# Optimization experiments

Measured on AMD Instinct MI355X. Metric: run time of the kernel, lower is better.

The kernel has to match this reference:

```python
import jax, jax.numpy as jnp
import numpy as np

B = 2048          # number of graphs
NPG = 128         # nodes per graph (hard-coded by lin1 = Linear(128*hid, 1))
N = B * NPG       # total nodes = 262144
DEG = 16          # avg degree
EPG = NPG * DEG   # edges per graph
E = B * EPG       # total edges = 4194304
IN_CH = 151
HID = 64


def setup_inputs() -> dict:
    key = jax.random.key(0)
    ks = jax.random.split(key, 6)
    x = jax.random.normal(ks[0], (N, IN_CH), jnp.float32)
    # within-graph random edges: local index in [0, NPG) plus per-graph node offset
    src_loc = jax.random.randint(ks[1], (E,), 0, NPG, dtype=jnp.int32)
    dst_loc = jax.random.randint(ks[2], (E,), 0, NPG, dtype=jnp.int32)
    off = ((jnp.arange(E, dtype=jnp.int32) // EPG) * NPG)
    edge_index = jnp.stack([src_loc + off, dst_loc + off])  # [2, E] int32
    edge_weight = jax.random.uniform(ks[3], (E,), jnp.float32)
    batch = jnp.arange(N, dtype=jnp.int32) // NPG  # sorted graph ids
    W1 = jax.random.normal(ks[4], (IN_CH, HID), jnp.float32) / np.sqrt(IN_CH)
    b1 = jnp.zeros((HID,), jnp.float32)
    Wlin = jax.random.normal(ks[5], (NPG * HID, 1), jnp.float32) / np.sqrt(NPG * HID)
    blin = jnp.zeros((1,), jnp.float32)
    return {"x": x, "edge_index": edge_index, "edge_weight": edge_weight,
            "batch": batch, "W1": W1, "b1": b1, "Wlin": Wlin, "blin": blin}


def _gcn_conv(x, row, col, w, W, b, num_nodes):
    # PyG GCNConv: h = x @ W; out[col] += dinv[row]*w*dinv[col] * h[row]; out += b
    h = x @ W                                        # [N, HID]
    deg = jax.ops.segment_sum(w, col, num_segments=num_nodes)
    dinv = jnp.where(deg > 0, jax.lax.rsqrt(deg), 0.0)
    norm = dinv[row] * w * dinv[col]                 # [E+N]
    out = jax.ops.segment_sum(h[row] * norm[:, None], col, num_segments=num_nodes)
    return out + b


def reference(x, edge_index, edge_weight, batch, W1, b1, Wlin, blin):
    num_nodes = x.shape[0]
    # add self-loops with weight 1 (GCNConv default)
    sl = jnp.arange(num_nodes, dtype=edge_index.dtype)
    row = jnp.concatenate([edge_index[0], sl])
    col = jnp.concatenate([edge_index[1], sl])
    w = jnp.concatenate([edge_weight, jnp.ones((num_nodes,), x.dtype)])
    h = jax.nn.relu(_gcn_conv(x, row, col, w, W1, b1, num_nodes))  # [N, HID]
    # linearize: nodes are batch-sorted, 128 per graph -> [B, 128*HID]
    g = h.reshape(num_nodes // NPG, NPG * h.shape[1])
    return jax.nn.sigmoid(g @ Wlin + blin)  # [B, 1]
```

## Files before the change

kernel.cpp:

```cpp
#include <hip/hip_runtime.h>
#include <math.h>

#define NPG 128
#define HID 64
#define ICH 151
#define EPG 2048
#define TPB 512
#define EPT (EPG / TPB)
#define KP  160
#define HTS 136
#define ASS 132
#define AS_OFF 17408

typedef __attribute__((ext_vector_type(8))) short  short8;
typedef __attribute__((ext_vector_type(4))) float  floatx4;

static __device__ __forceinline__ unsigned short f2bf(float v) {
    unsigned u = __builtin_bit_cast(unsigned, v);
    return (unsigned short)((u + 0x7fffu + ((u >> 16) & 1u)) >> 16);
}
static __device__ __forceinline__ unsigned packbf(float a, float b) {
    return (unsigned)f2bf(a) | ((unsigned)f2bf(b) << 16);
}
static __device__ __forceinline__ short8 pack8(const float* v) {
    union { unsigned u[4]; short8 s; } r;
    r.u[0] = packbf(v[0], v[1]);
    r.u[1] = packbf(v[2], v[3]);
    r.u[2] = packbf(v[4], v[5]);
    r.u[3] = packbf(v[6], v[7]);
    return r.s;
}

__global__ __launch_bounds__(512) void gcn_prep(const float* __restrict__ W1,
                                                short* __restrict__ W1T) {
    int i = threadIdx.x + blockIdx.x * 512;
    if (i < HID * KP) {
        int ch = i / KP, k = i - ch * KP;
        W1T[i] = (short)f2bf((k < ICH) ? W1[k * HID + ch] : 0.0f);
    }
}

__global__ __launch_bounds__(TPB, 6) void gcn_fused(
    const float* __restrict__ x,
    const int*   __restrict__ erow,
    const int*   __restrict__ ecol,
    const float* __restrict__ ew,
    const short* __restrict__ W1T,
    const float* __restrict__ b1,
    const float* __restrict__ Wlin,
    const float* __restrict__ blin,
    float* __restrict__ out)
{
    __shared__ __align__(16) char smem[AS_OFF + 64 * ASS * 4];
    __shared__ float deg[NPG];
    __shared__ float dinv[NPG];
    __shared__ float red[TPB / 64];

    short* ht = (short*)smem;
    float* As = (float*)(smem + AS_OFF);

    const int t    = threadIdx.x;
    const int g    = blockIdx.x;
    const int lane = t & 63;
    const int wv   = t >> 6;
    const int c16  = lane & 15;
    const int kq   = (lane >> 4) * 8;

    if (t < NPG) deg[t] = 1.0f;

    int   ep_[EPT];
    float nw_[EPT];
    const int ebase = g * EPG;
    #pragma unroll
    for (int it = 0; it < EPT; ++it) {
        int e = ebase + t + it * TPB;
        int rl = erow[e] & (NPG - 1);
        int cl = ecol[e] & (NPG - 1);
        ep_[it] = (cl << 7) | rl;
        nw_[it] = ew[e];
    }

    short8 af[5];
    {
        const float* xr = x + (size_t)g * (NPG * ICH) + (wv * 16 + c16) * ICH;
        #pragma unroll
        for (int s = 0; s < 5; ++s) {
            float v[8];
            #pragma unroll
            for (int j = 0; j < 8; ++j) {
                int k = s * 32 + kq + j;
                v[j] = (k < ICH) ? xr[k] : 0.0f;
            }
            af[s] = pack8(v);
        }
    }
    __syncthreads();

    #pragma unroll
    for (int it = 0; it < EPT; ++it)
        atomicAdd(&deg[ep_[it] >> 7], nw_[it]);

    #pragma unroll
    for (int n = 0; n < 4; ++n) {
        floatx4 acc = {0.0f, 0.0f, 0.0f, 0.0f};
        #pragma unroll
        for (int s = 0; s < 5; ++s) {
            short8 b = *(const short8*)&W1T[(n * 16 + c16) * KP + s * 32 + kq];
            acc = __builtin_amdgcn_mfma_f32_16x16x32_bf16(af[s], b, acc, 0, 0, 0);
        }
        int col = n * 16 + c16;
        int row = wv * 16 + (lane >> 4) * 4;
        *(int2*)&ht[col * HTS + row] =
            make_int2((int)packbf(acc[0], acc[1]), (int)packbf(acc[2], acc[3]));
    }
    __syncthreads();

    if (t < NPG) dinv[t] = rsqrtf(deg[t]);
    __syncthreads();

    #pragma unroll
    for (int it = 0; it < EPT; ++it) {
        int rl = ep_[it] & (NPG - 1), cl = ep_[it] >> 7;
        nw_[it] = dinv[rl] * nw_[it] * dinv[cl];
    }

    float partial = 0.0f;
    const int mrow = (wv >> 1) * 16 + c16;

    for (int half = 0; half < 2; ++half) {
        for (int p = t; p < 64 * ASS / 4; p += TPB)
            ((floatx4*)As)[p] = (floatx4){0.0f, 0.0f, 0.0f, 0.0f};
        __syncthreads();

        #pragma unroll
        for (int it = 0; it < EPT; ++it) {
            int cl = ep_[it] >> 7;
            if ((cl >> 6) == half)
                atomicAdd(&As[(cl & 63) * ASS + (ep_[it] & (NPG - 1))], nw_[it]);
        }
        if (t < 64) {
            int i = half * 64 + t;
            atomicAdd(&As[t * ASS + i], dinv[i] * dinv[i]);
        }
        __syncthreads();

        short8 afr[4];
        #pragma unroll
        for (int ks = 0; ks < 4; ++ks) {
            const float* ap = &As[mrow * ASS + ks * 32 + kq];
            floatx4 a0 = *(const floatx4*)ap;
            floatx4 a1 = *(const floatx4*)(ap + 4);
            float v[8] = {a0[0], a0[1], a0[2], a0[3], a1[0], a1[1], a1[2], a1[3]};
            afr[ks] = pack8(v);
        }
        #pragma unroll
        for (int nn = 0; nn < 2; ++nn) {
            int nt2 = (wv & 1) * 2 + nn;
            floatx4 acc = {0.0f, 0.0f, 0.0f, 0.0f};
            #pragma unroll
            for (int ks = 0; ks < 4; ++ks) {
                short8 b = *(const short8*)&ht[(nt2 * 16 + c16) * HTS + ks * 32 + kq];
                acc = __builtin_amdgcn_mfma_f32_16x16x32_bf16(afr[ks], b, acc, 0, 0, 0);
            }
            int col = nt2 * 16 + c16;
            float b1v = b1[col];
            int node0 = half * 64 + (wv >> 1) * 16 + (lane >> 4) * 4;
            #pragma unroll
            for (int r = 0; r < 4; ++r) {
                float v = fmaxf(acc[r] + b1v, 0.0f);
                partial += v * Wlin[(node0 + r) * HID + col];
            }
        }
        __syncthreads();
    }

    #pragma unroll
    for (int o = 32; o > 0; o >>= 1)
        partial += __shfl_down(partial, o, 64);
    if (lane == 0) red[wv] = partial;
    __syncthreads();
    if (t == 0) {
        float tot = blin[0];
        #pragma unroll
        for (int i = 0; i < TPB / 64; ++i) tot += red[i];
        out[g] = 1.0f / (1.0f + expf(-tot));
    }
}

extern "C" void kernel_launch(void* const* d_in, const int* in_sizes, int n_in,
                              void* d_out, int out_size, void* d_ws, size_t ws_size,
                              hipStream_t stream) {
    const float* x    = (const float*)d_in[0];
    const int*   ei   = (const int*)d_in[1];
    const float* ew   = (const float*)d_in[2];
    const float* W1   = (const float*)d_in[4];
    const float* b1   = (const float*)d_in[5];
    const float* Wlin = (const float*)d_in[6];
    const float* blin = (const float*)d_in[7];
    float* out = (float*)d_out;

    const int E = in_sizes[1] / 2;
    const int B = out_size;

    short* W1T = (short*)d_ws;

    gcn_prep<<<(HID * KP + 511) / 512, 512, 0, stream>>>(W1, W1T);
    gcn_fused<<<B, TPB, 0, stream>>>(x, ei, ei + E, ew, W1T, b1, Wlin, blin, out);
}
```

Baseline: 83.66 us.

## Split fused GCN kernel into separate feature GEMM and aggregation kernels

```diff
diff --git a/kernel.cpp b/kernel.cpp
--- a/kernel.cpp
+++ b/kernel.cpp
@@ -5,12 +5,10 @@
 #define HID 64
 #define ICH 151
 #define EPG 2048
-#define TPB 512
-#define EPT (EPG / TPB)
 #define KP  160
-#define HTS 136
 #define ASS 132
-#define AS_OFF 17408
+#define ATPB 512
+#define AEPT (EPG / ATPB)
 
 typedef __attribute__((ext_vector_type(8))) short  short8;
 typedef __attribute__((ext_vector_type(4))) float  floatx4;
@@ -40,49 +38,24 @@
     }
 }
 
-__global__ __launch_bounds__(TPB, 6) void gcn_fused(
+__global__ __launch_bounds__(256, 4) void gcn_gemm(
     const float* __restrict__ x,
-    const int*   __restrict__ erow,
-    const int*   __restrict__ ecol,
-    const float* __restrict__ ew,
     const short* __restrict__ W1T,
-    const float* __restrict__ b1,
-    const float* __restrict__ Wlin,
-    const float* __restrict__ blin,
-    float* __restrict__ out)
+    short* __restrict__ hg)
 {
-    __shared__ __align__(16) char smem[AS_OFF + 64 * ASS * 4];
-    __shared__ float deg[NPG];
-    __shared__ float dinv[NPG];
-    __shared__ float red[TPB / 64];
-
-    short* ht = (short*)smem;
-    float* As = (float*)(smem + AS_OFF);
-
     const int t    = threadIdx.x;
-    const int g    = blockIdx.x;
     const int lane = t & 63;
     const int wv   = t >> 6;
     const int c16  = lane & 15;
     const int kq   = (lane >> 4) * 8;
 
-    if (t < NPG) deg[t] = 1.0f;
-
-    int   ep_[EPT];
-    float nw_[EPT];
-    const int ebase = g * EPG;
-    #pragma unroll
-    for (int it = 0; it < EPT; ++it) {
-        int e = ebase + t + it * TPB;
-        int rl = erow[e] & (NPG - 1);
-        int cl = ecol[e] & (NPG - 1);
-        ep_[it] = (cl << 7) | rl;
-        nw_[it] = ew[e];
-    }
+    const int gw  = blockIdx.x * 4 + wv;
+    const int g   = gw >> 3;
+    const int sub = gw & 7;
 
     short8 af[5];
     {
-        const float* xr = x + (size_t)g * (NPG * ICH) + (wv * 16 + c16) * ICH;
+        const float* xr = x + ((size_t)g * NPG + sub * 16 + c16) * ICH;
         #pragma unroll
         for (int s = 0; s < 5; ++s) {
             float v[8];
@@ -94,12 +67,8 @@
             af[s] = pack8(v);
         }
     }
-    __syncthreads();
-
-    #pragma unroll
-    for (int it = 0; it < EPT; ++it)
-        atomicAdd(&deg[ep_[it] >> 7], nw_[it]);
-
+
+    short* hgg = hg + (size_t)g * (HID * NPG);
     #pragma unroll
     for (int n = 0; n < 4; ++n) {
         floatx4 acc = {0.0f, 0.0f, 0.0f, 0.0f};
@@ -109,31 +78,74 @@
             acc = __builtin_amdgcn_mfma_f32_16x16x32_bf16(af[s], b, acc, 0, 0, 0);
         }
         int col = n * 16 + c16;
-        int row = wv * 16 + (lane >> 4) * 4;
-        *(int2*)&ht[col * HTS + row] =
+        int row = sub * 16 + (lane >> 4) * 4;
+        *(int2*)&hgg[col * NPG + row] =
             make_int2((int)packbf(acc[0], acc[1]), (int)packbf(acc[2], acc[3]));
     }
+}
+
+__global__ __launch_bounds__(ATPB, 6) void gcn_agg(
+    const int*   __restrict__ erow,
+    const int*   __restrict__ ecol,
+    const float* __restrict__ ew,
+    const short* __restrict__ hg,
+    const float* __restrict__ b1,
+    const float* __restrict__ Wlin,
+    const float* __restrict__ blin,
+    float* __restrict__ out)
+{
+    __shared__ __align__(16) float As[64 * ASS];
+    __shared__ float deg[NPG];
+    __shared__ float dinv[NPG];
+    __shared__ float red[ATPB / 64];
+
+    const int t    = threadIdx.x;
+    const int g    = blockIdx.x;
+    const int lane = t & 63;
+    const int wv   = t >> 6;
+    const int c16  = lane & 15;
+    const int kq   = (lane >> 4) * 8;
+
+    if (t < NPG) deg[t] = 1.0f;
+
+    int   ep_[AEPT];
+    float nw_[AEPT];
+    const int ebase = g * EPG;
+    #pragma unroll
+    for (int it = 0; it < AEPT; ++it) {
+        int e = ebase + t + it * ATPB;
+        int rl = erow[e] & (NPG - 1);
+        int cl = ecol[e] & (NPG - 1);
+        ep_[it] = (cl << 7) | rl;
+        nw_[it] = ew[e];
+    }
+    __syncthreads();
+
+    #pragma unroll
+    for (int it = 0; it < AEPT; ++it)
+        atomicAdd(&deg[ep_[it] >> 7], nw_[it]);
     __syncthreads();
 
     if (t < NPG) dinv[t] = rsqrtf(deg[t]);
     __syncthreads();
 
     #pragma unroll
-    for (int it = 0; it < EPT; ++it) {
+    for (int it = 0; it < AEPT; ++it) {
         int rl = ep_[it] & (NPG - 1), cl = ep_[it] >> 7;
         nw_[it] = dinv[rl] * nw_[it] * dinv[cl];
     }
 
     float partial = 0.0f;
     const int mrow = (wv >> 1) * 16 + c16;
+    const short* hgg = hg + (size_t)g * (HID * NPG);
 
     for (int half = 0; half < 2; ++half) {
-        for (int p = t; p < 64 * ASS / 4; p += TPB)
+        for (int p = t; p < 64 * ASS / 4; p += ATPB)
             ((floatx4*)As)[p] = (floatx4){0.0f, 0.0f, 0.0f, 0.0f};
         __syncthreads();
 
         #pragma unroll
-        for (int it = 0; it < EPT; ++it) {
+        for (int it = 0; it < AEPT; ++it) {
             int cl = ep_[it] >> 7;
             if ((cl >> 6) == half)
                 atomicAdd(&As[(cl & 63) * ASS + (ep_[it] & (NPG - 1))], nw_[it]);
@@ -159,7 +171,7 @@
             floatx4 acc = {0.0f, 0.0f, 0.0f, 0.0f};
             #pragma unroll
             for (int ks = 0; ks < 4; ++ks) {
-                short8 b = *(const short8*)&ht[(nt2 * 16 + c16) * HTS + ks * 32 + kq];
+                short8 b = *(const short8*)&hgg[(nt2 * 16 + c16) * NPG + ks * 32 + kq];
                 acc = __builtin_amdgcn_mfma_f32_16x16x32_bf16(afr[ks], b, acc, 0, 0, 0);
             }
             int col = nt2 * 16 + c16;
@@ -182,7 +194,7 @@
     if (t == 0) {
         float tot = blin[0];
         #pragma unroll
-        for (int i = 0; i < TPB / 64; ++i) tot += red[i];
+        for (int i = 0; i < ATPB / 64; ++i) tot += red[i];
         out[g] = 1.0f / (1.0f + expf(-tot));
     }
 }
@@ -203,7 +215,9 @@
     const int B = out_size;
 
     short* W1T = (short*)d_ws;
+    short* hg  = (short*)d_ws + HID * KP;
 
     gcn_prep<<<(HID * KP + 511) / 512, 512, 0, stream>>>(W1, W1T);
-    gcn_fused<<<B, TPB, 0, stream>>>(x, ei, ei + E, ew, W1T, b1, Wlin, blin, out);
-}
+    gcn_gemm<<<B * 2, 256, 0, stream>>>(x, W1T, hg);
+    gcn_agg<<<B, ATPB, 0, stream>>>(ei, ei + E, ew, hg, b1, Wlin, blin, out);
+}
```

After: 133.8 us. 1.6x slower.

## Swizzle LDS layouts, hoist Wlin/b1 loads, and merge adjacency build with normalization

Applied to the files above, without the earlier changes.

```diff
diff --git a/kernel.cpp b/kernel.cpp
--- a/kernel.cpp
+++ b/kernel.cpp
@@ -8,9 +8,7 @@
 #define TPB 512
 #define EPT (EPG / TPB)
 #define KP  160
-#define HTS 136
-#define ASS 132
-#define AS_OFF 17408
+#define AS_OFF 16384
 
 typedef __attribute__((ext_vector_type(8))) short  short8;
 typedef __attribute__((ext_vector_type(4))) float  floatx4;
@@ -51,7 +49,7 @@
     const float* __restrict__ blin,
     float* __restrict__ out)
 {
-    __shared__ __align__(16) char smem[AS_OFF + 64 * ASS * 4];
+    __shared__ __align__(16) char smem[AS_OFF + 64 * 128 * 4];
     __shared__ float deg[NPG];
     __shared__ float dinv[NPG];
     __shared__ float red[TPB / 64];
@@ -80,6 +78,24 @@
         nw_[it] = ew[e];
     }
 
+    float wl[2][2][4];
+    float b1v[2];
+    {
+        const int rbase = (wv >> 1) * 16 + (lane >> 4) * 4;
+        #pragma unroll
+        for (int nn = 0; nn < 2; ++nn) {
+            int col = ((wv & 1) * 2 + nn) * 16 + c16;
+            b1v[nn] = b1[col];
+            #pragma unroll
+            for (int half = 0; half < 2; ++half) {
+                int node0 = half * 64 + rbase;
+                #pragma unroll
+                for (int r = 0; r < 4; ++r)
+                    wl[half][nn][r] = Wlin[(node0 + r) * HID + col];
+            }
+        }
+    }
+
     short8 af[5];
     {
         const float* xr = x + (size_t)g * (NPG * ICH) + (wv * 16 + c16) * ICH;
@@ -110,68 +126,79 @@
         }
         int col = n * 16 + c16;
         int row = wv * 16 + (lane >> 4) * 4;
-        *(int2*)&ht[col * HTS + row] =
+        *(int2*)&ht[col * 128 + (row ^ ((col & 7) << 3))] =
             make_int2((int)packbf(acc[0], acc[1]), (int)packbf(acc[2], acc[3]));
     }
     __syncthreads();
 
     if (t < NPG) dinv[t] = rsqrtf(deg[t]);
+    #pragma unroll
+    for (int p = 0; p < 4; ++p)
+        ((floatx4*)As)[t + p * TPB] = (floatx4){0.0f, 0.0f, 0.0f, 0.0f};
     __syncthreads();
 
     #pragma unroll
     for (int it = 0; it < EPT; ++it) {
         int rl = ep_[it] & (NPG - 1), cl = ep_[it] >> 7;
-        nw_[it] = dinv[rl] * nw_[it] * dinv[cl];
-    }
+        float nrm = dinv[rl] * nw_[it] * dinv[cl];
+        nw_[it] = nrm;
+        if ((cl >> 6) == 0)
+            atomicAdd(&As[(cl & 63) * 128 + (rl ^ ((cl & 7) << 2))], nrm);
+    }
+    if (t < 64)
+        atomicAdd(&As[t * 128 + (t ^ ((t & 7) << 2))], dinv[t] * dinv[t]);
+    __syncthreads();
 
     float partial = 0.0f;
     const int mrow = (wv >> 1) * 16 + c16;
+    const int msw  = (mrow & 7) << 2;
 
     for (int half = 0; half < 2; ++half) {
-        for (int p = t; p < 64 * ASS / 4; p += TPB)
-            ((floatx4*)As)[p] = (floatx4){0.0f, 0.0f, 0.0f, 0.0f};
-        __syncthreads();
-
-        #pragma unroll
-        for (int it = 0; it < EPT; ++it) {
-            int cl = ep_[it] >> 7;
-            if ((cl >> 6) == half)
-                atomicAdd(&As[(cl & 63) * ASS + (ep_[it] & (NPG - 1))], nw_[it]);
-        }
-        if (t < 64) {
-            int i = half * 64 + t;
-            atomicAdd(&As[t * ASS + i], dinv[i] * dinv[i]);
-        }
-        __syncthreads();
-
         short8 afr[4];
         #pragma unroll
         for (int ks = 0; ks < 4; ++ks) {
-            const float* ap = &As[mrow * ASS + ks * 32 + kq];
-            floatx4 a0 = *(const floatx4*)ap;
-            floatx4 a1 = *(const floatx4*)(ap + 4);
+            int r0 = ks * 32 + kq;
+            floatx4 a0 = *(const floatx4*)&As[mrow * 128 + (r0 ^ msw)];
+            floatx4 a1 = *(const floatx4*)&As[mrow * 128 + ((r0 + 4) ^ msw)];
             float v[8] = {a0[0], a0[1], a0[2], a0[3], a1[0], a1[1], a1[2], a1[3]};
             afr[ks] = pack8(v);
         }
         #pragma unroll
         for (int nn = 0; nn < 2; ++nn) {
-            int nt2 = (wv & 1) * 2 + nn;
+            int ch = ((wv & 1) * 2 + nn) * 16 + c16;
+            int hsw = (ch & 7) << 3;
             floatx4 acc = {0.0f, 0.0f, 0.0f, 0.0f};
             #pragma unroll
             for (int ks = 0; ks < 4; ++ks) {
-                short8 b = *(const short8*)&ht[(nt2 * 16 + c16) * HTS + ks * 32 + kq];
+                short8 b = *(const short8*)&ht[ch * 128 + ((ks * 32 + kq) ^ hsw)];
                 acc = __builtin_amdgcn_mfma_f32_16x16x32_bf16(afr[ks], b, acc, 0, 0, 0);
             }
-            int col = nt2 * 16 + c16;
-            float b1v = b1[col];
-            int node0 = half * 64 + (wv >> 1) * 16 + (lane >> 4) * 4;
             #pragma unroll
             for (int r = 0; r < 4; ++r) {
-                float v = fmaxf(acc[r] + b1v, 0.0f);
-                partial += v * Wlin[(node0 + r) * HID + col];
-            }
-        }
-        __syncthreads();
+                float v = fmaxf(acc[r] + b1v[nn], 0.0f);
+                partial += v * wl[half][nn][r];
+            }
+        }
+
+        if (half == 0) {
+            __syncthreads();
+            #pragma unroll
+            for (int p = 0; p < 4; ++p)
+                ((floatx4*)As)[t + p * TPB] = (floatx4){0.0f, 0.0f, 0.0f, 0.0f};
+            __syncthreads();
+
+            #pragma unroll
+            for (int it = 0; it < EPT; ++it) {
+                int rl = ep_[it] & (NPG - 1), cl = ep_[it] >> 7;
+                if ((cl >> 6) == 1)
+                    atomicAdd(&As[(cl & 63) * 128 + (rl ^ ((cl & 7) << 2))], nw_[it]);
+            }
+            if (t < 64) {
+                int i = 64 + t;
+                atomicAdd(&As[t * 128 + (i ^ ((t & 7) << 2))], dinv[i] * dinv[i]);
+            }
+            __syncthreads();
+        }
     }
 
     #pragma unroll
```

New measurement: 102.4 us. 1.22x slower.

## Accumulate raw edge weights into bf16 adjacency in one pass, defer normalization

Applied to the files above, without the earlier changes.

```diff
diff --git a/kernel.cpp b/kernel.cpp
--- a/kernel.cpp
+++ b/kernel.cpp
@@ -9,8 +9,8 @@
 #define EPT (EPG / TPB)
 #define KP  160
 #define HTS 136
-#define ASS 132
-#define AS_OFF 17408
+#define ABS 136
+#define AB_OFF 17408
 
 typedef __attribute__((ext_vector_type(8))) short  short8;
 typedef __attribute__((ext_vector_type(4))) float  floatx4;
@@ -18,6 +18,9 @@
 static __device__ __forceinline__ unsigned short f2bf(float v) {
     unsigned u = __builtin_bit_cast(unsigned, v);
     return (unsigned short)((u + 0x7fffu + ((u >> 16) & 1u)) >> 16);
+}
+static __device__ __forceinline__ float bf2f(short b) {
+    return __builtin_bit_cast(float, ((unsigned)(unsigned short)b) << 16);
 }
 static __device__ __forceinline__ unsigned packbf(float a, float b) {
     return (unsigned)f2bf(a) | ((unsigned)f2bf(b) << 16);
@@ -29,6 +32,19 @@
     r.u[2] = packbf(v[4], v[5]);
     r.u[3] = packbf(v[6], v[7]);
     return r.s;
+}
+
+static __device__ __forceinline__ void lds_bf16_add(short* base, int idx, float w) {
+    unsigned* a = (unsigned*)base + (idx >> 1);
+    unsigned sh = (unsigned)(idx & 1) << 4;
+    unsigned cur = *(volatile unsigned*)a;
+    for (;;) {
+        unsigned old = cur;
+        float f = __builtin_bit_cast(float, ((old >> sh) & 0xFFFFu) << 16) + w;
+        unsigned nw2 = (old & ~(0xFFFFu << sh)) | ((unsigned)f2bf(f) << sh);
+        cur = atomicCAS(a, old, nw2);
+        if (cur == old) break;
+    }
 }
 
 __global__ __launch_bounds__(512) void gcn_prep(const float* __restrict__ W1,
@@ -51,13 +67,12 @@
     const float* __restrict__ blin,
     float* __restrict__ out)
 {
-    __shared__ __align__(16) char smem[AS_OFF + 64 * ASS * 4];
+    __shared__ __align__(16) char smem[AB_OFF + NPG * ABS * 2];
     __shared__ float deg[NPG];
-    __shared__ float dinv[NPG];
     __shared__ float red[TPB / 64];
 
     short* ht = (short*)smem;
-    float* As = (float*)(smem + AS_OFF);
+    short* Ab = (short*)(smem + AB_OFF);
 
     const int t    = threadIdx.x;
     const int g    = blockIdx.x;
@@ -67,6 +82,18 @@
     const int kq   = (lane >> 4) * 8;
 
     if (t < NPG) deg[t] = 1.0f;
+    {
+        for (int p = t; p < NPG * ABS / 8; p += TPB) {
+            union { int4 i4; short s[8]; } c;
+            c.i4 = make_int4(0, 0, 0, 0);
+            int i = (8 * p + 136) / 137;
+            int d = i * 137 - 8 * p;
+            if (i < NPG && d >= 0 && d < 8)
+                c.s[d] = (short)0x3F80;
+            *(int4*)&Ab[p * 8] = c.i4;
+        }
+    }
+    __syncthreads();
 
     int   ep_[EPT];
     float nw_[EPT];
@@ -94,11 +121,13 @@
             af[s] = pack8(v);
         }
     }
-    __syncthreads();
-
-    #pragma unroll
-    for (int it = 0; it < EPT; ++it)
-        atomicAdd(&deg[ep_[it] >> 7], nw_[it]);
+
+    #pragma unroll
+    for (int it = 0; it < EPT; ++it) {
+        int rl = ep_[it] & (NPG - 1), cl = ep_[it] >> 7;
+        atomicAdd(&deg[cl], nw_[it]);
+        lds_bf16_add(Ab, cl * ABS + rl, nw_[it]);
+    }
 
     #pragma unroll
     for (int n = 0; n < 4; ++n) {
@@ -115,63 +144,40 @@
     }
     __syncthreads();
 
-    if (t < NPG) dinv[t] = rsqrtf(deg[t]);
-    __syncthreads();
-
-    #pragma unroll
-    for (int it = 0; it < EPT; ++it) {
-        int rl = ep_[it] & (NPG - 1), cl = ep_[it] >> 7;
-        nw_[it] = dinv[rl] * nw_[it] * dinv[cl];
-    }
+    const int arow  = wv * 16 + c16;
+    const int rbase = wv * 16 + (lane >> 4) * 4;
+
+    short8 afr[4];
+    #pragma unroll
+    for (int ks = 0; ks < 4; ++ks) {
+        short8 a = *(const short8*)&Ab[arow * ABS + ks * 32 + kq];
+        float v[8];
+        #pragma unroll
+        for (int j = 0; j < 8; ++j)
+            v[j] = bf2f(a[j]) * rsqrtf(deg[ks * 32 + kq + j]);
+        afr[ks] = pack8(v);
+    }
+    float rs[4];
+    #pragma unroll
+    for (int r = 0; r < 4; ++r)
+        rs[r] = rsqrtf(deg[rbase + r]);
 
     float partial = 0.0f;
-    const int mrow = (wv >> 1) * 16 + c16;
-
-    for (int half = 0; half < 2; ++half) {
-        for (int p = t; p < 64 * ASS / 4; p += TPB)
-            ((floatx4*)As)[p] = (floatx4){0.0f, 0.0f, 0.0f, 0.0f};
-        __syncthreads();
-
-        #pragma unroll
-        for (int it = 0; it < EPT; ++it) {
-            int cl = ep_[it] >> 7;
-            if ((cl >> 6) == half)
-                atomicAdd(&As[(cl & 63) * ASS + (ep_[it] & (NPG - 1))], nw_[it]);
-        }
-        if (t < 64) {
-            int i = half * 64 + t;
-            atomicAdd(&As[t * ASS + i], dinv[i] * dinv[i]);
-        }
-        __syncthreads();
-
-        short8 afr[4];
+    #pragma unroll
+    for (int nt = 0; nt < 4; ++nt) {
+        int col = nt * 16 + c16;
+        floatx4 acc = {0.0f, 0.0f, 0.0f, 0.0f};
         #pragma unroll
         for (int ks = 0; ks < 4; ++ks) {
-            const float* ap = &As[mrow * ASS + ks * 32 + kq];
-            floatx4 a0 = *(const floatx4*)ap;
-            floatx4 a1 = *(const floatx4*)(ap + 4);
-            float v[8] = {a0[0], a0[1], a0[2], a0[3], a1[0], a1[1], a1[2], a1[3]};
-            afr[ks] = pack8(v);
-        }
-        #pragma unroll
-        for (int nn = 0; nn < 2; ++nn) {
-            int nt2 = (wv & 1) * 2 + nn;
-            floatx4 acc = {0.0f, 0.0f, 0.0f, 0.0f};
-            #pragma unroll
-            for (int ks = 0; ks < 4; ++ks) {
-                short8 b = *(const short8*)&ht[(nt2 * 16 + c16) * HTS + ks * 32 + kq];
-                acc = __builtin_amdgcn_mfma_f32_16x16x32_bf16(afr[ks], b, acc, 0, 0, 0);
-            }
-            int col = nt2 * 16 + c16;
-            float b1v = b1[col];
-            int node0 = half * 64 + (wv >> 1) * 16 + (lane >> 4) * 4;
-            #pragma unroll
-            for (int r = 0; r < 4; ++r) {
-                float v = fmaxf(acc[r] + b1v, 0.0f);
-                partial += v * Wlin[(node0 + r) * HID + col];
-            }
-        }
-        __syncthreads();
+            short8 b = *(const short8*)&ht[col * HTS + ks * 32 + kq];
+            acc = __builtin_amdgcn_mfma_f32_16x16x32_bf16(afr[ks], b, acc, 0, 0, 0);
+        }
+        float b1v = b1[col];
+        #pragma unroll
+        for (int r = 0; r < 4; ++r) {
+            float v = fmaxf(acc[r] * rs[r] + b1v, 0.0f);
+            partial += v * Wlin[(rbase + r) * HID + col];
+        }
     }
 
     #pragma unroll
```

After: 83.88 us. Within noise of the previous version (+0.3%).
